# Performance work log

Measured on AMD Instinct MI355X. Metric: run time of the kernel, lower is better.

Reference implementation:

```python
import jax, jax.numpy as jnp
import numpy as np
from jax import lax

# QuantumDMRGLayer (isolated_labelnode=True) as a pure MPS chain contraction.
# Per sample: contract each site's (2,m[,m]) tensor with the 2-dim input vector
# over the physical leg, then multiply the resulting bond matrices along the
# chain, inserting the (m,m,nblabels) output tensor after site pos_label.

B, L, M, NBL = 2048, 196, 16, 10  # batch, dimvec, bond_len, nblabels


def setup_inputs() -> dict:
    key = jax.random.key(0)
    k_in, k_mid, k_l, k_r, k_out = jax.random.split(key, 5)
    # std chosen for numerical stability of a 196-long matrix product:
    # each site matrix is x0*A[0]+x1*A[1] with x~N(0,1), so effective per-site
    # gain ~ std*sqrt(2*m); std = 1/sqrt(2*m) keeps the product O(1).
    std = 1.0 / np.sqrt(2.0 * M)
    inputs = jax.random.normal(k_in, (B, L, 2), dtype=jnp.float32)
    eye2m = jnp.eye(M, dtype=jnp.float32)[:2, :]  # eye(max(2,m))[0:2,:] -> (2, m)
    A_left = eye2m + 1e-3 * jax.random.normal(k_l, (2, M), dtype=jnp.float32)
    A_right = eye2m + 1e-3 * jax.random.normal(k_r, (2, M), dtype=jnp.float32)
    A_mid = std * jax.random.normal(k_mid, (L - 2, 2, M, M), dtype=jnp.float32)
    T_out = (1.0 / np.sqrt(M)) * jax.random.normal(k_out, (M, M, NBL), dtype=jnp.float32)
    return {
        "inputs": inputs,
        "A_left": A_left,
        "A_mid": A_mid,
        "A_right": A_right,
        "T_out": T_out,
        "pos_label": 98,
    }


def reference(inputs, A_left, A_mid, A_right, T_out, pos_label):
    # Contract physical legs: interior site i (1..L-2) -> batched (m,m) matrix.
    mats = jnp.einsum("bsd,sdij->sbij", inputs[:, 1:-1, :], A_mid)  # (L-2, B, m, m)
    v_left = jnp.einsum("bd,dm->bm", inputs[:, 0, :], A_left)       # (B, m)
    v_right = jnp.einsum("bd,dm->bm", inputs[:, -1, :], A_right)    # (B, m)

    def step_l(v, Mx):  # v @ M, batched
        return jnp.einsum("bm,bmn->bn", v, Mx), None

    def step_r(v, Mx):  # M @ v, batched (sweep from the right end inward)
        return jnp.einsum("bmn,bn->bm", Mx, v), None

    # sites 1..pos_label feed the left bond of the output node,
    # sites pos_label+1..L-2 feed the right bond.
    left, _ = lax.scan(step_l, v_left, mats[:pos_label])
    right, _ = lax.scan(step_r, v_right, mats[pos_label:], reverse=True)
    return jnp.einsum("bm,mnl,bn->bl", left, T_out, right)  # (B, nblabels)
```

## Files before the change

kernel.cpp:

```cpp
#include <hip/hip_runtime.h>


#define XR 392
#define MROW 20
#define MATF 320
#define CHF 2560

#define SWZ_STEP(r, e0, e1)                                                    \
    { float vv = __int_as_float(__builtin_amdgcn_ds_swizzle(                   \
          __float_as_int(v), 0x1F | ((r) << 10)));                             \
      acc0 = fmaf(vv, (e0), acc0); acc1 = fmaf(vv, (e1), acc1); }

__global__ __launch_bounds__(128)
void QuantumDMRGLayer_kernel(const float* __restrict__ X,
                             const float* __restrict__ AL,
                             const float* __restrict__ AM,
                             const float* __restrict__ AR,
                             const float* __restrict__ T,
                             float* __restrict__ OUT)
{
    __shared__ float sA[2][2][CHF];
    __shared__ float sX[4 * XR];
    __shared__ float sT[2560];
    __shared__ float sV[4][2][16];

    const int tid  = threadIdx.x;
    const int wv   = tid >> 6;
    const int lane = tid & 63;
    const int g    = lane >> 4;
    const int n    = lane & 15;
    const int b0   = (int)blockIdx.x << 2;

    for (int k = tid; k < 4 * 98; k += 128) {
        const int smp = k / 98, w = k - smp * 98;
        const float4 v4 = ((const float4*)(X + (size_t)(b0 + smp) * XR))[w];
        ((float4*)(sX + smp * XR))[w] = v4;
    }
    for (int k = tid; k < 640; k += 128)
        ((float4*)sT)[k] = ((const float4*)T)[k];

    float4 st[8];

    auto stage_load = [&](int cc) {
#pragma unroll
        for (int k = 0; k < 4; ++k) {
            const int flat = k * 128 + tid;
            const int sl   = flat >> 7;
            const int rem  = flat & 127;
            const int idxL = cc * 4 + sl;
            const int idxR = 193 - (cc * 4 + sl);
            st[k]     = ((const float4*)AM)[idxL * 128 + rem];
            st[4 + k] = ((const float4*)AM)[idxR * 128 + rem];
        }
    };
    auto stage_write = [&](int buf) {
#pragma unroll
        for (int k = 0; k < 4; ++k) {
            const int flat = k * 128 + tid;
            const int sl = flat >> 7, rem = flat & 127;
            const int d = rem >> 6, m = (rem >> 2) & 15, q = rem & 3;
            const int base = (sl * 2 + d) * MATF;
            const float lv[4] = { st[k].x, st[k].y, st[k].z, st[k].w };
            const float rv[4] = { st[4+k].x, st[4+k].y, st[4+k].z, st[4+k].w };
#pragma unroll
            for (int i = 0; i < 4; ++i) {
                const int nn = q * 4 + i;
                const int r  = m ^ nn;
                sA[buf][0][base + nn * MROW + r] = lv[i];
                sA[buf][1][base + m  * MROW + r] = rv[i];
            }
        }
    };

    stage_load(0);
    stage_write(0);
    __syncthreads();

    const float* Ab = (wv == 0) ? AL : AR;
    const float2 x0 = *(const float2*)(sX + g * XR + (wv == 0 ? 0 : 390));
    float v = x0.x * Ab[n] + x0.y * Ab[16 + n];

    const int lim = (wv == 0) ? 98 : 96;
    for (int c = 0; c < 25; ++c) {
        if (c < 24) stage_load(c + 1);
        const float* As = sA[c & 1][wv];
#pragma unroll
        for (int j = 0; j < 4; ++j) {
            const int idx = c * 4 + j;
            if (idx >= lim) break;
            const int xo = (wv == 0) ? (2 + 2 * idx) : (2 * (194 - idx));
            const float2 xs = *(const float2*)(sX + g * XR + xo);
            const float* r0 = As + (j * 2) * MATF + n * MROW;
            const float* r1 = r0 + MATF;
            const float4 A0 = *(const float4*)(r0);
            const float4 A1 = *(const float4*)(r0 + 4);
            const float4 A2 = *(const float4*)(r0 + 8);
            const float4 A3 = *(const float4*)(r0 + 12);
            const float4 B0 = *(const float4*)(r1);
            const float4 B1 = *(const float4*)(r1 + 4);
            const float4 B2 = *(const float4*)(r1 + 8);
            const float4 B3 = *(const float4*)(r1 + 12);
            float acc0 = v * A0.x;
            float acc1 = v * B0.x;
            SWZ_STEP(1,  A0.y, B0.y)
            SWZ_STEP(2,  A0.z, B0.z)
            SWZ_STEP(3,  A0.w, B0.w)
            SWZ_STEP(4,  A1.x, B1.x)
            SWZ_STEP(5,  A1.y, B1.y)
            SWZ_STEP(6,  A1.z, B1.z)
            SWZ_STEP(7,  A1.w, B1.w)
            SWZ_STEP(8,  A2.x, B2.x)
            SWZ_STEP(9,  A2.y, B2.y)
            SWZ_STEP(10, A2.z, B2.z)
            SWZ_STEP(11, A2.w, B2.w)
            SWZ_STEP(12, A3.x, B3.x)
            SWZ_STEP(13, A3.y, B3.y)
            SWZ_STEP(14, A3.z, B3.z)
            SWZ_STEP(15, A3.w, B3.w)
            v = fmaf(xs.x, acc0, xs.y * acc1);
        }
        if (c < 24) stage_write((c + 1) & 1);
        __syncthreads();
    }

    sV[g][wv][n] = v;
    __syncthreads();
    if (tid < 40) {
        const int sm = tid / 10;
        const int l  = tid - sm * 10;
        const float* Rv = &sV[sm][1][0];
        const float4 Ra = *(const float4*)(Rv);
        const float4 Rb = *(const float4*)(Rv + 4);
        const float4 Rc = *(const float4*)(Rv + 8);
        const float4 Rd = *(const float4*)(Rv + 12);
        float acc = 0.f;
#pragma unroll
        for (int m = 0; m < 16; ++m) {
            const float lm = sV[sm][0][m];
            const float* Tp = sT + m * 160 + l;
            acc = fmaf(lm * Ra.x, Tp[0],   acc);
            acc = fmaf(lm * Ra.y, Tp[10],  acc);
            acc = fmaf(lm * Ra.z, Tp[20],  acc);
            acc = fmaf(lm * Ra.w, Tp[30],  acc);
            acc = fmaf(lm * Rb.x, Tp[40],  acc);
            acc = fmaf(lm * Rb.y, Tp[50],  acc);
            acc = fmaf(lm * Rb.z, Tp[60],  acc);
            acc = fmaf(lm * Rb.w, Tp[70],  acc);
            acc = fmaf(lm * Rc.x, Tp[80],  acc);
            acc = fmaf(lm * Rc.y, Tp[90],  acc);
            acc = fmaf(lm * Rc.z, Tp[100], acc);
            acc = fmaf(lm * Rc.w, Tp[110], acc);
            acc = fmaf(lm * Rd.x, Tp[120], acc);
            acc = fmaf(lm * Rd.y, Tp[130], acc);
            acc = fmaf(lm * Rd.z, Tp[140], acc);
            acc = fmaf(lm * Rd.w, Tp[150], acc);
        }
        OUT[(b0 + sm) * 10 + l] = acc;
    }
}

extern "C" void kernel_launch(void* const* d_in, const int* in_sizes, int n_in,
                              void* d_out, int out_size, void* d_ws, size_t ws_size,
                              hipStream_t stream)
{
    const float* X  = (const float*)d_in[0];
    const float* AL = (const float*)d_in[1];
    const float* AM = (const float*)d_in[2];
    const float* AR = (const float*)d_in[3];
    const float* T  = (const float*)d_in[4];
    (void)in_sizes; (void)n_in; (void)out_size; (void)d_ws; (void)ws_size;
    float* OUT = (float*)d_out;
    hipLaunchKernelGGL(QuantumDMRGLayer_kernel, dim3(512), dim3(128), 0, stream,
                       X, AL, AM, AR, T, OUT);
}
```

Measured before the change: 102.9 us.

## Pre-permute site tensors into workspace and stream them directly into registers

A new pre-kernel rewrites the interior site tensors into a per-lane rotated layout in the workspace, so each lane of the main kernel reads its 16-element rows straight from global memory (through cache) into registers. This removes the LDS double-buffer staging and the per-chunk __syncthreads. The cross-lane broadcast switches from ds_swizzle to DPP row rotates, and the final contraction reads T from global instead of LDS. The cost is an extra kernel launch and higher register pressure, and every step now depends on global or L2 load latency, hidden only by a two-site register prefetch.

Measured after the change: 112.2 us. +9.0%, slower.

```diff
diff --git a/kernel.cpp b/kernel.cpp
--- a/kernel.cpp
+++ b/kernel.cpp
@@ -2,26 +2,39 @@
 
 
 #define XR 392
-#define MROW 20
-#define MATF 320
-#define CHF 2560
+#define SITE_F 512
+#define STRM_F (100 * SITE_F)
 
-#define SWZ_STEP(r, e0, e1)                                                    \
-    { float vv = __int_as_float(__builtin_amdgcn_ds_swizzle(                   \
-          __float_as_int(v), 0x1F | ((r) << 10)));                             \
-      acc0 = fmaf(vv, (e0), acc0); acc1 = fmaf(vv, (e1), acc1); }
+#define DPPV(r) __int_as_float(__builtin_amdgcn_update_dpp(                    \
+    __float_as_int(v), __float_as_int(v), 0x120 + (r), 0xF, 0xF, false))
+
+__global__ __launch_bounds__(256)
+void perm_kernel(const float* __restrict__ AM, float* __restrict__ WS)
+{
+    const int bid = blockIdx.x;
+    const int tid = threadIdx.x;
+    const int n = tid >> 4, r = tid & 15;
+    const int k = (bid < 196) ? bid : bid - 196;
+    const int strm = (bid < 196) ? 0 : 1;
+    const int p = k >> 1, d = k & 1;
+    float val;
+    if (strm == 0) {
+        val = AM[p * 512 + d * 256 + ((n - r) & 15) * 16 + n];
+    } else {
+        val = AM[(193 - p) * 512 + d * 256 + n * 16 + ((n - r) & 15)];
+    }
+    WS[strm * STRM_F + p * SITE_F + d * 256 + tid] = val;
+}
 
 __global__ __launch_bounds__(128)
 void QuantumDMRGLayer_kernel(const float* __restrict__ X,
                              const float* __restrict__ AL,
-                             const float* __restrict__ AM,
                              const float* __restrict__ AR,
                              const float* __restrict__ T,
+                             const float* __restrict__ WS,
                              float* __restrict__ OUT)
 {
-    __shared__ float sA[2][2][CHF];
     __shared__ float sX[4 * XR];
-    __shared__ float sT[2560];
     __shared__ float sV[4][2][16];
 
     const int tid  = threadIdx.x;
@@ -36,91 +49,60 @@
         const float4 v4 = ((const float4*)(X + (size_t)(b0 + smp) * XR))[w];
         ((float4*)(sX + smp * XR))[w] = v4;
     }
-    for (int k = tid; k < 640; k += 128)
-        ((float4*)sT)[k] = ((const float4*)T)[k];
-
-    float4 st[8];
-
-    auto stage_load = [&](int cc) {
-#pragma unroll
-        for (int k = 0; k < 4; ++k) {
-            const int flat = k * 128 + tid;
-            const int sl   = flat >> 7;
-            const int rem  = flat & 127;
-            const int idxL = cc * 4 + sl;
-            const int idxR = 193 - (cc * 4 + sl);
-            st[k]     = ((const float4*)AM)[idxL * 128 + rem];
-            st[4 + k] = ((const float4*)AM)[idxR * 128 + rem];
-        }
-    };
-    auto stage_write = [&](int buf) {
-#pragma unroll
-        for (int k = 0; k < 4; ++k) {
-            const int flat = k * 128 + tid;
-            const int sl = flat >> 7, rem = flat & 127;
-            const int d = rem >> 6, m = (rem >> 2) & 15, q = rem & 3;
-            const int base = (sl * 2 + d) * MATF;
-            const float lv[4] = { st[k].x, st[k].y, st[k].z, st[k].w };
-            const float rv[4] = { st[4+k].x, st[4+k].y, st[4+k].z, st[4+k].w };
-#pragma unroll
-            for (int i = 0; i < 4; ++i) {
-                const int nn = q * 4 + i;
-                const int r  = m ^ nn;
-                sA[buf][0][base + nn * MROW + r] = lv[i];
-                sA[buf][1][base + m  * MROW + r] = rv[i];
-            }
-        }
-    };
-
-    stage_load(0);
-    stage_write(0);
     __syncthreads();
 
     const float* Ab = (wv == 0) ? AL : AR;
     const float2 x0 = *(const float2*)(sX + g * XR + (wv == 0 ? 0 : 390));
     float v = x0.x * Ab[n] + x0.y * Ab[16 + n];
 
+    const float* Pb = WS + (wv ? STRM_F : 0) + n * 16;
+    const float* xg = sX + g * XR;
+
+    float4 QA[8], QB[8];
+    auto load_site = [&](float4* Q, int p) {
+        const float* rp = Pb + p * SITE_F;
+        Q[0] = *(const float4*)(rp);
+        Q[1] = *(const float4*)(rp + 4);
+        Q[2] = *(const float4*)(rp + 8);
+        Q[3] = *(const float4*)(rp + 12);
+        Q[4] = *(const float4*)(rp + 256);
+        Q[5] = *(const float4*)(rp + 260);
+        Q[6] = *(const float4*)(rp + 264);
+        Q[7] = *(const float4*)(rp + 268);
+    };
+    auto step = [&](const float4* Q, int p) {
+        const int xo = (wv == 0) ? (2 + 2 * p) : (388 - 2 * p);
+        const float2 xs = *(const float2*)(xg + xo);
+        const float t1 = DPPV(1),  t2 = DPPV(2),  t3 = DPPV(3),  t4 = DPPV(4);
+        const float t5 = DPPV(5),  t6 = DPPV(6),  t7 = DPPV(7),  t8 = DPPV(8);
+        const float t9 = DPPV(9),  t10 = DPPV(10), t11 = DPPV(11), t12 = DPPV(12);
+        const float t13 = DPPV(13), t14 = DPPV(14), t15 = DPPV(15);
+        float a0 = v * Q[0].x;                 float b0 = v * Q[4].x;
+        float a1 = t1 * Q[0].y;                float b1 = t1 * Q[4].y;
+        a0 = fmaf(t2,  Q[0].z, a0);            b0 = fmaf(t2,  Q[4].z, b0);
+        a1 = fmaf(t3,  Q[0].w, a1);            b1 = fmaf(t3,  Q[4].w, b1);
+        a0 = fmaf(t4,  Q[1].x, a0);            b0 = fmaf(t4,  Q[5].x, b0);
+        a1 = fmaf(t5,  Q[1].y, a1);            b1 = fmaf(t5,  Q[5].y, b1);
+        a0 = fmaf(t6,  Q[1].z, a0);            b0 = fmaf(t6,  Q[5].z, b0);
+        a1 = fmaf(t7,  Q[1].w, a1);            b1 = fmaf(t7,  Q[5].w, b1);
+        a0 = fmaf(t8,  Q[2].x, a0);            b0 = fmaf(t8,  Q[6].x, b0);
+        a1 = fmaf(t9,  Q[2].y, a1);            b1 = fmaf(t9,  Q[6].y, b1);
+        a0 = fmaf(t10, Q[2].z, a0);            b0 = fmaf(t10, Q[6].z, b0);
+        a1 = fmaf(t11, Q[2].w, a1);            b1 = fmaf(t11, Q[6].w, b1);
+        a0 = fmaf(t12, Q[3].x, a0);            b0 = fmaf(t12, Q[7].x, b0);
+        a1 = fmaf(t13, Q[3].y, a1);            b1 = fmaf(t13, Q[7].y, b1);
+        a0 = fmaf(t14, Q[3].z, a0);            b0 = fmaf(t14, Q[7].z, b0);
+        a1 = fmaf(t15, Q[3].w, a1);            b1 = fmaf(t15, Q[7].w, b1);
+        v = fmaf(xs.x, a0 + a1, xs.y * (b0 + b1));
+    };
+
     const int lim = (wv == 0) ? 98 : 96;
-    for (int c = 0; c < 25; ++c) {
-        if (c < 24) stage_load(c + 1);
-        const float* As = sA[c & 1][wv];
-#pragma unroll
-        for (int j = 0; j < 4; ++j) {
-            const int idx = c * 4 + j;
-            if (idx >= lim) break;
-            const int xo = (wv == 0) ? (2 + 2 * idx) : (2 * (194 - idx));
-            const float2 xs = *(const float2*)(sX + g * XR + xo);
-            const float* r0 = As + (j * 2) * MATF + n * MROW;
-            const float* r1 = r0 + MATF;
-            const float4 A0 = *(const float4*)(r0);
-            const float4 A1 = *(const float4*)(r0 + 4);
-            const float4 A2 = *(const float4*)(r0 + 8);
-            const float4 A3 = *(const float4*)(r0 + 12);
-            const float4 B0 = *(const float4*)(r1);
-            const float4 B1 = *(const float4*)(r1 + 4);
-            const float4 B2 = *(const float4*)(r1 + 8);
-            const float4 B3 = *(const float4*)(r1 + 12);
-            float acc0 = v * A0.x;
-            float acc1 = v * B0.x;
-            SWZ_STEP(1,  A0.y, B0.y)
-            SWZ_STEP(2,  A0.z, B0.z)
-            SWZ_STEP(3,  A0.w, B0.w)
-            SWZ_STEP(4,  A1.x, B1.x)
-            SWZ_STEP(5,  A1.y, B1.y)
-            SWZ_STEP(6,  A1.z, B1.z)
-            SWZ_STEP(7,  A1.w, B1.w)
-            SWZ_STEP(8,  A2.x, B2.x)
-            SWZ_STEP(9,  A2.y, B2.y)
-            SWZ_STEP(10, A2.z, B2.z)
-            SWZ_STEP(11, A2.w, B2.w)
-            SWZ_STEP(12, A3.x, B3.x)
-            SWZ_STEP(13, A3.y, B3.y)
-            SWZ_STEP(14, A3.z, B3.z)
-            SWZ_STEP(15, A3.w, B3.w)
-            v = fmaf(xs.x, acc0, xs.y * acc1);
-        }
-        if (c < 24) stage_write((c + 1) & 1);
-        __syncthreads();
+    load_site(QA, 0);
+    for (int p = 0; p < lim; p += 2) {
+        load_site(QB, p + 1);
+        step(QA, p);
+        load_site(QA, p + 2);
+        step(QB, p + 1);
     }
 
     sV[g][wv][n] = v;
@@ -137,7 +119,7 @@
 #pragma unroll
         for (int m = 0; m < 16; ++m) {
             const float lm = sV[sm][0][m];
-            const float* Tp = sT + m * 160 + l;
+            const float* Tp = T + m * 160 + l;
             acc = fmaf(lm * Ra.x, Tp[0],   acc);
             acc = fmaf(lm * Ra.y, Tp[10],  acc);
             acc = fmaf(lm * Ra.z, Tp[20],  acc);
@@ -168,8 +150,11 @@
     const float* AM = (const float*)d_in[2];
     const float* AR = (const float*)d_in[3];
     const float* T  = (const float*)d_in[4];
-    (void)in_sizes; (void)n_in; (void)out_size; (void)d_ws; (void)ws_size;
+    (void)in_sizes; (void)n_in; (void)out_size; (void)ws_size;
+    float* WS  = (float*)d_ws;
     float* OUT = (float*)d_out;
+
+    hipLaunchKernelGGL(perm_kernel, dim3(388), dim3(256), 0, stream, AM, WS);
     hipLaunchKernelGGL(QuantumDMRGLayer_kernel, dim3(512), dim3(128), 0, stream,
-                       X, AL, AM, AR, T, OUT);
+                       X, AL, AR, T, WS, OUT);
 }
```
